# Performance work log

Hardware: AMD Instinct MI355X
Metric: run time of the kernel (lower is better)

## Reference

```python
import jax, jax.numpy as jnp
import numpy as np

T = 4096          # flattened document length (tokens)
FLAT = 512        # 2 * lstm_hidden_size
HD = 256          # head embedding dim (head_emb + char_emb)
FEAT = 20         # feature_size
MAXW = 20         # max mention width
NCAND = 30000     # enumerated candidate spans
HID = 512         # scorer hidden size
K = 1638          # floor(T * ment_ratio=0.4)
C = 40            # max antecedents
DEPTH = 2         # coref_depth
NSPK = 10
MENT = 2 * FLAT + FEAT + HD        # 1300 mention emb size
BIN_WIDTHS = [1, 1, 1, 1, 1, 4, 8, 16, 32]   # sums to 65 -> covers clamp(dist,0,64)
BINS = jnp.asarray(np.concatenate([np.full(w, i, dtype=np.int32) for i, w in enumerate(BIN_WIDTHS)]))


def _scorer(x, w1, b1, w2, b2, w3, b3):
    h = jax.nn.relu(x @ w1 + b1)
    h = jax.nn.relu(h @ w2 + b2)
    return (h @ w3 + b3)[..., 0]


def setup_inputs():
    key = jax.random.key(0)
    ks = jax.random.split(key, 30)
    p = lambda i, s: jax.random.normal(ks[i], s, jnp.float32) * 0.02
    cand_starts = jax.random.randint(ks[25], (NCAND,), 0, T)
    widths = jax.random.randint(ks[26], (NCAND,), 0, MAXW)
    cand_ends = jnp.minimum(cand_starts + widths, T - 1)
    return {
        "flat_lstm_out": jax.random.normal(ks[0], (T, FLAT), jnp.float32),
        "head_doc_embs": jax.random.normal(ks[1], (T, HD), jnp.float32),
        "w_span_head": p(2, (FLAT,)), "b_span_head": jnp.zeros((), jnp.float32),
        "width_embed": p(3, (MAXW, FEAT)),
        "ms_w1": p(4, (MENT, HID)), "ms_b1": jnp.zeros((HID,), jnp.float32),
        "ms_w2": p(5, (HID, HID)), "ms_b2": jnp.zeros((HID,), jnp.float32),
        "ms_w3": p(6, (HID, 1)), "ms_b3": jnp.zeros((1,), jnp.float32),
        "fast_w": p(7, (MENT, MENT)), "fast_b": jnp.zeros((MENT,), jnp.float32),
        "ss_w1": p(8, (3 * MENT + 3 * FEAT, HID)), "ss_b1": jnp.zeros((HID,), jnp.float32),
        "ss_w2": p(9, (HID, HID)), "ss_b2": jnp.zeros((HID,), jnp.float32),
        "ss_w3": p(10, (HID, 1)), "ss_b3": jnp.zeros((1,), jnp.float32),
        "gate_w": p(11, (2 * MENT, MENT)), "gate_b": jnp.zeros((MENT,), jnp.float32),
        "speaker_embed": p(12, (2, FEAT)),
        "genre_embed": p(13, (7, FEAT)),
        "dist_embed": p(14, (len(BIN_WIDTHS), FEAT)),
        "cand_starts": cand_starts,
        "cand_ends": cand_ends,
        "speaker_ids": jax.random.randint(ks[27], (T,), 0, NSPK),
        "genre_id": 3,
    }


def reference(flat_lstm_out, head_doc_embs, w_span_head, b_span_head, width_embed,
              ms_w1, ms_b1, ms_w2, ms_b2, ms_w3, ms_b3, fast_w, fast_b,
              ss_w1, ss_b1, ss_w2, ss_b2, ss_w3, ss_b3, gate_w, gate_b,
              speaker_embed, genre_embed, dist_embed,
              cand_starts, cand_ends, speaker_ids, genre_id):
    neg = -jnp.inf
    # ---- mention (span) embeddings: start/end gather + width emb + attention-pooled head ----
    width = cand_ends - cand_starts + 1                              # [N]
    start_embs = flat_lstm_out[cand_starts]                          # [N,FLAT]
    end_embs = flat_lstm_out[cand_ends]                              # [N,FLAT]
    width_embs = width_embed[width - 1]                              # [N,FEAT]
    span_idxs = jnp.clip(jnp.arange(MAXW)[None, :] + cand_starts[:, None], 0, T - 1)  # [N,W]
    ment_doc = head_doc_embs[span_idxs]                              # [N,W,HD]
    head_scores = flat_lstm_out @ w_span_head + b_span_head          # [T]
    g = head_scores[span_idxs] + jnp.where(jnp.arange(MAXW)[None, :] < width[:, None], 0.0, neg)
    attn = jax.nn.softmax(g, axis=1)                                 # [N,W]
    head_embs = jnp.einsum('nw,nwd->nd', attn, ment_doc)             # [N,HD]
    cand_embs = jnp.concatenate([start_embs, end_embs, width_embs, head_embs], axis=1)  # [N,MENT]
    cand_scores = _scorer(cand_embs, ms_w1, ms_b1, ms_w2, ms_b2, ms_w3, ms_b3)          # [N]
    # ---- prune mentions: top-k by score, reordered by document position ----
    _, top_idx = jax.lax.top_k(cand_scores, K)
    ment_pos = cand_starts[top_idx] * cand_ends[-1] + cand_ends[top_idx]
    top_idx = top_idx[jnp.argsort(ment_pos)]
    ment_embs = cand_embs[top_idx]                                   # [K,MENT]
    ment_scores = cand_scores[top_idx]                               # [K]
    ment_speakers = speaker_ids[cand_starts[top_idx]]                # [K]
    # ---- fast (bilinear) antecedent scoring + top-c pruning ----
    idx = jnp.arange(K)
    mask = (idx[:, None] - idx[None, :]) > 0                         # antecedent must precede
    src = ment_embs @ fast_w + fast_b
    fast = src @ ment_embs.T + ment_scores[:, None] + ment_scores[None, :] + jnp.where(mask, 0.0, neg)
    top_fast, antes = jax.lax.top_k(fast, C)                         # [K,C]
    dummy = jnp.zeros((K, 1), fast.dtype)
    genre_emb = jnp.broadcast_to(genre_embed[genre_id][None, None, :], (K, C, FEAT))
    ante_scores = top_fast
    # ---- iterative slow antecedent scoring + gated refinement ----
    for _ in range(DEPTH):
        ante_ment = ment_embs[antes]                                 # [K,C,MENT]
        same = (ment_speakers[:, None] == ment_speakers[antes]).astype(jnp.int32)
        spk_emb = speaker_embed[same]                                # [K,C,FEAT]
        dist_bin = BINS[jnp.clip(idx[:, None] - antes, 0, 64)]
        dist_emb = dist_embed[dist_bin]                              # [K,C,FEAT]
        me = jnp.broadcast_to(ment_embs[:, None, :], (K, C, MENT))
        ante_emb = jnp.concatenate([me, ante_ment, ante_ment * me, spk_emb, genre_emb, dist_emb], axis=2)
        ante_scores = top_fast + _scorer(ante_emb, ss_w1, ss_b1, ss_w2, ss_b2, ss_w3, ss_b3)
        weights = jax.nn.softmax(jnp.concatenate([dummy, ante_scores], axis=1), axis=-1)  # [K,C+1]
        stacked = jnp.concatenate([ment_embs[:, None, :], ante_ment], axis=1)             # [K,C+1,MENT]
        attended = jnp.einsum('kc,kcd->kd', weights, stacked)
        f = jax.nn.sigmoid(jnp.concatenate([ment_embs, attended], axis=1) @ gate_w + gate_b)
        ment_embs = f * attended + (1.0 - f) * ment_embs
    return jnp.concatenate([dummy, ante_scores], axis=1)             # [K,C+1] coref logits
```

## Files before the change

### kernel.cpp

```cpp
#include <hip/hip_runtime.h>
#include <math.h>

#define T_LEN 4096
#define FLATD 512
#define HDD 256
#define FEATD 20
#define NCAND 30000
#define HIDD 512
#define KSEL 1638
#define CANT 40
#define MENTD 1300
#define KPAD 1312
#define NPAIR (KSEL*CANT)
#define NEG_INF (-__builtin_inff())

#define MF_RELU 1
#define MF_MASK 4
#define MF_GATE 8

typedef unsigned short u16;
typedef __attribute__((ext_vector_type(8))) short bf16x8;
typedef __attribute__((ext_vector_type(4))) float f32x4;

__device__ __forceinline__ unsigned ordf(float f){
  unsigned u = __float_as_uint(f);
  return (u & 0x80000000u) ? ~u : (u | 0x80000000u);
}
__device__ __forceinline__ float unordf(unsigned u){
  return __uint_as_float((u & 0x80000000u) ? (u ^ 0x80000000u) : ~u);
}
__device__ __forceinline__ float bf2f(u16 h){ return __uint_as_float(((unsigned)h) << 16); }
__device__ __forceinline__ u16 f2bf(float f){
  unsigned u = __float_as_uint(f);
  u += 0x7fffu + ((u >> 16) & 1u);
  return (u16)(u >> 16);
}
__device__ __forceinline__ unsigned pkmul(unsigned a, unsigned b){
  float a0 = __uint_as_float(a << 16), a1 = __uint_as_float(a & 0xffff0000u);
  float b0 = __uint_as_float(b << 16), b1 = __uint_as_float(b & 0xffff0000u);
  float p0 = a0*b0, p1 = a1*b1;
  unsigned r;
  asm("v_cvt_pk_bf16_f32 %0, %1, %2" : "=v"(r) : "v"(p0), "v"(p1));
  return r;
}
__device__ __forceinline__ int featsrc(int k){
  if (k < 1024) return k;
  if (k < 1280) return k + 20;
  if (k < 1300) return k - 256;
  return -1;
}
__device__ __forceinline__ int swz(int row, int k8){
  return row*32 + ((k8 ^ ((row >> 1) & 3)) << 3);
}
__device__ __forceinline__ void gload16(const u16* g, u16* l){
  __builtin_amdgcn_global_load_lds((const __attribute__((address_space(1))) void*)(g),
                                   (__attribute__((address_space(3))) void*)(l), 16, 0, 0);
}

__global__ __launch_bounds__(256) void k_prep(const float* __restrict__ flat,
    const float* __restrict__ wemb, const float* __restrict__ fast_b, const float* __restrict__ gate_b,
    u16* __restrict__ flatbf, u16* __restrict__ wembP, float* __restrict__ fbP, float* __restrict__ gbP,
    unsigned* __restrict__ selws)
{
  int i = blockIdx.x*256 + threadIdx.x;
  if (i < T_LEN*FLATD) flatbf[i] = f2bf(flat[i]);
  if (i < 20*32) wembP[i] = ((i & 31) < 20) ? f2bf(wemb[(i >> 5)*FEATD + (i & 31)]) : (u16)0;
  if (i < KPAD){
    int s = featsrc(i);
    fbP[i] = (s >= 0) ? fast_b[s] : 0.f;
    gbP[i] = (s >= 0) ? gate_b[s] : 0.f;
  }
  if (i < 6156) selws[i] = 0;
}

__global__ __launch_bounds__(256) void k_head(const float* __restrict__ flat,
    const float* __restrict__ w, const float* __restrict__ b, float* __restrict__ hs)
{
  int lane = threadIdx.x & 63, wid = threadIdx.x >> 6;
  int row = blockIdx.x*4 + wid;
  if (row >= T_LEN) return;
  const float* x = flat + (size_t)row*FLATD;
  float s = 0.f;
  for (int j = lane; j < FLATD; j += 64) s += x[j]*w[j];
  #pragma unroll
  for (int o = 32; o; o >>= 1) s += __shfl_down(s, o, 64);
  if (lane == 0) hs[row] = s + b[0];
}

__global__ __launch_bounds__(256) void k_cand(const float* __restrict__ hs,
    const float* __restrict__ hdoc, const int* __restrict__ starts, const int* __restrict__ ends,
    u16* __restrict__ hemb)
{
  int wid = threadIdx.x >> 6, lane = threadIdx.x & 63;
  int n = blockIdx.x*4 + wid;
  if (n >= NCAND) return;
  int s = starts[n], e = ends[n];
  int width = e - s + 1;
  float g[20];
  #pragma unroll
  for (int w2 = 0; w2 < 20; ++w2) g[w2] = (w2 < width) ? hs[min(s + w2, T_LEN-1)] : NEG_INF;
  float m = NEG_INF;
  #pragma unroll
  for (int w2 = 0; w2 < 20; ++w2) m = fmaxf(m, g[w2]);
  float sum = 0.f;
  #pragma unroll
  for (int w2 = 0; w2 < 20; ++w2){ g[w2] = expf(g[w2] - m); sum += g[w2]; }
  float inv = 1.f/sum;
  #pragma unroll
  for (int di = 0; di < 4; ++di){
    int d = lane + di*64;
    float acc = 0.f;
    #pragma unroll
    for (int w2 = 0; w2 < 20; ++w2)
      acc += g[w2]*hdoc[(size_t)min(s + w2, T_LEN-1)*HDD + d];
    hemb[(size_t)n*HDD + d] = f2bf(acc*inv);
  }
}

__global__ __launch_bounds__(256) void k_transall(const float* __restrict__ ms_w1,
    const float* __restrict__ ms_w2, const float* __restrict__ fast_w,
    const float* __restrict__ ss_w1, const float* __restrict__ ss_w2,
    const float* __restrict__ gate_w,
    u16* ms1T, u16* ms2T, u16* fastT, u16* ss1abT, u16* sspT,
    u16* ss2T, u16* gateTall)
{
  const float* B; u16* D; int Kb, N, srcN, ldD, kperm, nperm;
  switch (blockIdx.z){
    case 0: B = ms_w1; D = ms1T; Kb = KPAD; N = HIDD; srcN = HIDD; ldD = KPAD; kperm = 1; nperm = 0; break;
    case 1: B = ms_w2; D = ms2T; Kb = HIDD; N = HIDD; srcN = HIDD; ldD = HIDD; kperm = 0; nperm = 0; break;
    case 2: B = fast_w; D = fastT; Kb = KPAD; N = MENTD; srcN = MENTD; ldD = KPAD; kperm = 1; nperm = 1; break;
    case 3: B = ss_w1; D = ss1abT; Kb = KPAD; N = HIDD; srcN = HIDD; ldD = KPAD; kperm = 1; nperm = 0; break;
    case 4: B = ss_w1 + (size_t)MENTD*HIDD; D = ss1abT + (size_t)512*KPAD; Kb = KPAD; N = HIDD; srcN = HIDD; ldD = KPAD; kperm = 1; nperm = 0; break;
    case 5: B = ss_w1 + (size_t)2*MENTD*HIDD; D = sspT; Kb = KPAD; N = HIDD; srcN = HIDD; ldD = KPAD; kperm = 1; nperm = 0; break;
    case 6: B = ss_w2; D = ss2T; Kb = HIDD; N = HIDD; srcN = HIDD; ldD = HIDD; kperm = 0; nperm = 0; break;
    case 7: B = gate_w; D = gateTall; Kb = KPAD; N = MENTD; srcN = MENTD; ldD = 2*KPAD; kperm = 1; nperm = 1; break;
    default: B = gate_w + (size_t)MENTD*MENTD; D = gateTall + KPAD; Kb = KPAD; N = MENTD; srcN = MENTD; ldD = 2*KPAD; kperm = 1; nperm = 1; break;
  }
  int k0 = blockIdx.x*32, n0 = blockIdx.y*32;
  if (k0 >= Kb || n0 >= N) return;
  __shared__ float t[32][33];
  int tx = threadIdx.x & 31, ty = threadIdx.x >> 5;
  for (int r = ty; r < 32; r += 8){
    int gk = k0 + r, gn = n0 + tx;
    int sk = kperm ? featsrc(gk) : ((gk < Kb) ? gk : -1);
    int sn = nperm ? ((gn < N) ? featsrc(gn) : -1) : ((gn < N) ? gn : -1);
    t[r][tx] = (sk >= 0 && sn >= 0) ? B[(size_t)sk*srcN + sn] : 0.f;
  }
  __syncthreads();
  for (int r = ty; r < 32; r += 8){
    int gn = n0 + r, gk = k0 + tx;
    if (gn < N && gk < Kb) D[(size_t)gn*ldD + gk] = f2bf(t[tx][r]);
  }
}

__global__ __launch_bounds__(256) void k_mfma_cand(
    const u16* __restrict__ flatbf, const u16* __restrict__ hemb, const u16* __restrict__ wembP,
    const int* __restrict__ starts, const int* __restrict__ ends,
    const u16* __restrict__ Bt, int M, const float* __restrict__ bias, u16* __restrict__ Cbf)
{
  __shared__ alignas(16) u16 As[4096];
  __shared__ alignas(16) u16 Bs[4096];
  int tid = threadIdx.x;
  int row0 = blockIdx.y*128, col0 = blockIdx.x*128;
  int lane = tid & 63, wid = tid >> 6;
  int wr = wid >> 1, wc = wid & 1;
  int l15 = lane & 15, l4 = lane >> 4;

  int s0 = tid, s1 = tid + 256;
  int r0s = s0 >> 2, c0s = s0 & 3;
  int r1s = s1 >> 2, c1s = s1 & 3;
  int k80 = (c0s ^ ((r0s >> 1) & 3)) << 3;
  int k81 = (c1s ^ ((r1s >> 1) & 3)) << 3;
  int n0r = row0 + r0s; if (n0r >= M) n0r = M - 1;
  int n1r = row0 + r1s; if (n1r >= M) n1r = M - 1;
  int sA0 = starts[n0r], eA0 = ends[n0r];
  int sA1 = starts[n1r], eA1 = ends[n1r];
  const u16* bS0 = flatbf + (size_t)sA0*FLATD;
  const u16* bE0 = flatbf + (size_t)eA0*FLATD;
  const u16* bH0 = hemb + (size_t)n0r*HDD;
  const u16* bW0 = wembP + (eA0 - sA0)*32;
  const u16* bS1 = flatbf + (size_t)sA1*FLATD;
  const u16* bE1 = flatbf + (size_t)eA1*FLATD;
  const u16* bH1p = hemb + (size_t)n1r*HDD;
  const u16* bW1 = wembP + (eA1 - sA1)*32;
  const u16* pb0 = Bt + (size_t)(col0 + r0s)*KPAD + k80;
  const u16* pb1 = Bt + (size_t)(col0 + r1s)*KPAD + k81;
  u16* la0 = As + s0*8; u16* la1 = As + s1*8;
  u16* lb0 = Bs + s0*8; u16* lb1 = Bs + s1*8;

  f32x4 acc[4][4];
  #pragma unroll
  for (int m = 0; m < 4; ++m)
    #pragma unroll
    for (int n = 0; n < 4; ++n)
      #pragma unroll
      for (int q = 0; q < 4; ++q) acc[m][n][q] = 0.f;

  for (int kt = 0; kt < KPAD/32; ++kt){
    int k0 = kt << 5;
    int f0 = k0 + k80, f1 = k0 + k81;
    const u16* src0 = (f0 < 512) ? bS0 + f0 : (f0 < 1024) ? bE0 + (f0 - 512)
                    : (f0 < 1280) ? bH0 + (f0 - 1024) : bW0 + (f0 - 1280);
    const u16* src1 = (f1 < 512) ? bS1 + f1 : (f1 < 1024) ? bE1 + (f1 - 512)
                    : (f1 < 1280) ? bH1p + (f1 - 1024) : bW1 + (f1 - 1280);
    gload16(src0, la0); gload16(src1, la1);
    gload16(pb0 + k0, lb0); gload16(pb1 + k0, lb1);
    __syncthreads();
    bf16x8 af[4], bfr[4];
    #pragma unroll
    for (int m = 0; m < 4; ++m){ int r = wr*64 + m*16 + l15; af[m] = *(const bf16x8*)(As + swz(r, l4)); }
    #pragma unroll
    for (int n = 0; n < 4; ++n){ int cc = wc*64 + n*16 + l15; bfr[n] = *(const bf16x8*)(Bs + swz(cc, l4)); }
    #pragma unroll
    for (int m = 0; m < 4; ++m)
      #pragma unroll
      for (int n = 0; n < 4; ++n)
        acc[m][n] = __builtin_amdgcn_mfma_f32_16x16x32_bf16(af[m], bfr[n], acc[m][n], 0, 0, 0);
    __syncthreads();
  }
  #pragma unroll
  for (int m = 0; m < 4; ++m){
    #pragma unroll
    for (int q = 0; q < 4; ++q){
      int grow = row0 + wr*64 + m*16 + l4*4 + q;
      if (grow >= M) continue;
      #pragma unroll
      for (int n = 0; n < 4; ++n){
        int gcol = col0 + wc*64 + n*16 + l15;
        float v = fmaxf(acc[m][n][q] + bias[gcol], 0.f);
        Cbf[(size_t)grow*HIDD + gcol] = f2bf(v);
      }
    }
  }
}

__global__ __launch_bounds__(256) void k_mfma(const u16* __restrict__ A,
    const u16* __restrict__ A2, const u16* __restrict__ Bt, int M, int N, int Kp, int ldA,
    const float* __restrict__ bias, const float* __restrict__ msc,
    float* __restrict__ Cf, int ldf, u16* __restrict__ Cbf, int ldbf, int Nstore, int flags,
    const u16* __restrict__ g_att, const u16* __restrict__ g_mo)
{
  __shared__ alignas(16) u16 As[4096];
  __shared__ alignas(16) u16 Bs[4096];
  int tid = threadIdx.x;
  int row0 = blockIdx.y*128, col0 = blockIdx.x*128;
  if ((flags & MF_MASK) && col0 >= row0 + 128) return;
  int lane = tid & 63, wid = tid >> 6;
  int wr = wid >> 1, wc = wid & 1;
  int l15 = lane & 15, l4 = lane >> 4;

  int s0 = tid, s1 = tid + 256;
  int r0s = s0 >> 2, c0s = s0 & 3;
  int r1s = s1 >> 2, c1s = s1 & 3;
  int k80 = (c0s ^ ((r0s >> 1) & 3)) << 3;
  int k81 = (c1s ^ ((r1s >> 1) & 3)) << 3;
  int ra0 = row0 + r0s; if (ra0 >= M) ra0 = M - 1;
  int ra1 = row0 + r1s; if (ra1 >= M) ra1 = M - 1;
  int cb0 = col0 + r0s; if (cb0 >= N) cb0 = N - 1;
  int cb1 = col0 + r1s; if (cb1 >= N) cb1 = N - 1;
  const u16* pa0 = A + (size_t)ra0*ldA + k80;
  const u16* pa1 = A + (size_t)ra1*ldA + k81;
  int kt1 = A2 ? (ldA >> 5) : (Kp >> 5);
  int koff = kt1 << 5;
  const u16* qa0 = A2 ? (A2 + (size_t)ra0*ldA + k80 - koff) : pa0;
  const u16* qa1 = A2 ? (A2 + (size_t)ra1*ldA + k81 - koff) : pa1;
  const u16* pb0 = Bt + (size_t)cb0*Kp + k80;
  const u16* pb1 = Bt + (size_t)cb1*Kp + k81;
  u16* la0 = As + s0*8; u16* la1 = As + s1*8;
  u16* lb0 = Bs + s0*8; u16* lb1 = Bs + s1*8;

  f32x4 acc[4][4];
  #pragma unroll
  for (int m = 0; m < 4; ++m)
    #pragma unroll
    for (int n = 0; n < 4; ++n)
      #pragma unroll
      for (int q = 0; q < 4; ++q) acc[m][n][q] = 0.f;

  int nkt = Kp >> 5;
  for (int kt = 0; kt < nkt; ++kt){
    int k0 = kt << 5;
    const u16* a0 = (kt < kt1) ? pa0 : qa0;
    const u16* a1 = (kt < kt1) ? pa1 : qa1;
    gload16(a0 + k0, la0); gload16(a1 + k0, la1);
    gload16(pb0 + k0, lb0); gload16(pb1 + k0, lb1);
    __syncthreads();
    bf16x8 af[4], bfr[4];
    #pragma unroll
    for (int m = 0; m < 4; ++m){ int r = wr*64 + m*16 + l15; af[m] = *(const bf16x8*)(As + swz(r, l4)); }
    #pragma unroll
    for (int n = 0; n < 4; ++n){ int cc = wc*64 + n*16 + l15; bfr[n] = *(const bf16x8*)(Bs + swz(cc, l4)); }
    #pragma unroll
    for (int m = 0; m < 4; ++m)
      #pragma unroll
      for (int n = 0; n < 4; ++n)
        acc[m][n] = __builtin_amdgcn_mfma_f32_16x16x32_bf16(af[m], bfr[n], acc[m][n], 0, 0, 0);
    __syncthreads();
  }
  #pragma unroll
  for (int m = 0; m < 4; ++m){
    #pragma unroll
    for (int q = 0; q < 4; ++q){
      int grow = row0 + wr*64 + m*16 + l4*4 + q;
      if (grow >= M) continue;
      #pragma unroll
      for (int n = 0; n < 4; ++n){
        int gcol = col0 + wc*64 + n*16 + l15;
        if (gcol < N){
          float v = acc[m][n][q];
          if (bias) v += bias[gcol];
          if (flags & MF_MASK){ v += msc[grow] + msc[gcol]; if (gcol >= grow) v = NEG_INF; }
          if (flags & MF_RELU) v = fmaxf(v, 0.f);
          if (flags & MF_GATE){
            float f = 1.f/(1.f + expf(-v));
            float res = f*bf2f(g_att[(size_t)grow*ldbf + gcol])
                      + (1.f - f)*bf2f(g_mo[(size_t)grow*ldbf + gcol]);
            Cbf[(size_t)grow*ldbf + gcol] = f2bf(res);
          } else {
            if (Cf)  Cf[(size_t)grow*ldf + gcol] = v;
            if (Cbf) Cbf[(size_t)grow*ldbf + gcol] = f2bf(v);
          }
        } else if (Cbf && gcol < Nstore){
          Cbf[(size_t)grow*ldbf + gcol] = 0;
        }
      }
    }
  }
}

__global__ __launch_bounds__(256) void k_mfma_rowdot(const u16* __restrict__ A,
    const u16* __restrict__ Bt, int M, const float* __restrict__ b2,
    const float* __restrict__ w3, const float* __restrict__ b3,
    const float* __restrict__ add, float* __restrict__ out)
{
  __shared__ alignas(16) u16 As[4096];
  __shared__ alignas(16) u16 Bs[4096];
  __shared__ float rsum[128][2];
  int tid = threadIdx.x;
  int row0 = blockIdx.x*128;
  int lane = tid & 63, wid = tid >> 6;
  int wr = wid >> 1, wc = wid & 1;
  int l15 = lane & 15, l4 = lane >> 4;

  int s0 = tid, s1 = tid + 256;
  int r0s = s0 >> 2, c0s = s0 & 3;
  int r1s = s1 >> 2, c1s = s1 & 3;
  int k80 = (c0s ^ ((r0s >> 1) & 3)) << 3;
  int k81 = (c1s ^ ((r1s >> 1) & 3)) << 3;
  int ra0 = row0 + r0s; if (ra0 >= M) ra0 = M - 1;
  int ra1 = row0 + r1s; if (ra1 >= M) ra1 = M - 1;
  const u16* pa0 = A + (size_t)ra0*HIDD + k80;
  const u16* pa1 = A + (size_t)ra1*HIDD + k81;
  u16* la0 = As + s0*8; u16* la1 = As + s1*8;
  u16* lb0 = Bs + s0*8; u16* lb1 = Bs + s1*8;

  float rd[4][4] = {};
  for (int p = 0; p < 4; ++p){
    int col0 = p*128;
    const u16* pb0 = Bt + (size_t)(col0 + r0s)*HIDD + k80;
    const u16* pb1 = Bt + (size_t)(col0 + r1s)*HIDD + k81;
    f32x4 acc[4][4];
    #pragma unroll
    for (int m = 0; m < 4; ++m)
      #pragma unroll
      for (int n = 0; n < 4; ++n)
        #pragma unroll
        for (int q = 0; q < 4; ++q) acc[m][n][q] = 0.f;
    for (int kt = 0; kt < HIDD/32; ++kt){
      int k0 = kt << 5;
      gload16(pa0 + k0, la0); gload16(pa1 + k0, la1);
      gload16(pb0 + k0, lb0); gload16(pb1 + k0, lb1);
      __syncthreads();
      bf16x8 af[4], bfr[4];
      #pragma unroll
      for (int m = 0; m < 4; ++m){ int r = wr*64 + m*16 + l15; af[m] = *(const bf16x8*)(As + swz(r, l4)); }
      #pragma unroll
      for (int n = 0; n < 4; ++n){ int cc = wc*64 + n*16 + l15; bfr[n] = *(const bf16x8*)(Bs + swz(cc, l4)); }
      #pragma unroll
      for (int m = 0; m < 4; ++m)
        #pragma unroll
        for (int n = 0; n < 4; ++n)
          acc[m][n] = __builtin_amdgcn_mfma_f32_16x16x32_bf16(af[m], bfr[n], acc[m][n], 0, 0, 0);
      __syncthreads();
    }
    #pragma unroll
    for (int n = 0; n < 4; ++n){
      int gcol = col0 + wc*64 + n*16 + l15;
      float bb = b2[gcol], ww = w3[gcol];
      #pragma unroll
      for (int m = 0; m < 4; ++m)
        #pragma unroll
        for (int q = 0; q < 4; ++q){
          float v = fmaxf(acc[m][n][q] + bb, 0.f);
          rd[m][q] = fmaf(v, ww, rd[m][q]);
        }
    }
  }
  #pragma unroll
  for (int m = 0; m < 4; ++m)
    #pragma unroll
    for (int q = 0; q < 4; ++q){
      float s = rd[m][q];
      s += __shfl_xor(s, 1, 64); s += __shfl_xor(s, 2, 64);
      s += __shfl_xor(s, 4, 64); s += __shfl_xor(s, 8, 64);
      if (l15 == 0) rsum[wr*64 + m*16 + l4*4 + q][wc] = s;
    }
  __syncthreads();
  if (tid < 128){
    int gr = row0 + tid;
    if (gr < M){
      float v = rsum[tid][0] + rsum[tid][1] + b3[0];
      if (add) v += add[gr];
      out[gr] = v;
    }
  }
}

__global__ __launch_bounds__(256) void k_d1_mfma(int Mc,
    const u16* __restrict__ ment, const int* __restrict__ antes, const int* __restrict__ mspk,
    const u16* __restrict__ Bt, const float* __restrict__ A_meb,
    const float* __restrict__ comb, u16* __restrict__ H1)
{
  __shared__ alignas(16) u16 As[4096];
  __shared__ alignas(16) u16 Bs[8192];
  __shared__ int ri[128], rj[128], rcomb[128];
  int tid = threadIdx.x;
  int row0 = blockIdx.y*128;
  int col0 = blockIdx.x*256;
  if (tid < 128){
    int r = row0 + tid;
    int p = (r < Mc ? r : 0);
    int i = p / CANT;
    int j = antes[p];
    ri[tid] = i; rj[tid] = j;
    int same = (mspk[i] == mspk[j]) ? 1 : 0;
    int d = i - j; d = d < 0 ? 0 : (d > 64 ? 64 : d);
    int bin = (d <= 4) ? d : (d <= 8 ? 5 : (d <= 16 ? 6 : (d <= 32 ? 7 : 8)));
    rcomb[tid] = same*9 + bin;
  }
  __syncthreads();
  int lane = tid & 63, wid = tid >> 6;
  int wr = wid >> 1, wc = wid & 1;
  int l15 = lane & 15, l4 = lane >> 4;

  int s0 = tid, s1 = tid + 256;
  int r0s = s0 >> 2, c0s = s0 & 3;
  int r1s = s1 >> 2, c1s = s1 & 3;
  int k80 = (c0s ^ ((r0s >> 1) & 3)) << 3;
  int k81 = (c1s ^ ((r1s >> 1) & 3)) << 3;
  const u16* pi0 = ment + (size_t)ri[r0s]*KPAD + k80;
  const u16* pj0 = ment + (size_t)rj[r0s]*KPAD + k80;
  const u16* pi1 = ment + (size_t)ri[r1s]*KPAD + k81;
  const u16* pj1 = ment + (size_t)rj[r1s]*KPAD + k81;
  int t0 = tid, t1 = tid + 256, t2 = tid + 512, t3 = tid + 768;
  int rB0 = t0 >> 2, rB1 = t1 >> 2, rB2 = t2 >> 2, rB3 = t3 >> 2;
  int kB0 = ((t0 & 3) ^ ((rB0 >> 1) & 3)) << 3;
  int kB1 = ((t1 & 3) ^ ((rB1 >> 1) & 3)) << 3;
  int kB2 = ((t2 & 3) ^ ((rB2 >> 1) & 3)) << 3;
  int kB3 = ((t3 & 3) ^ ((rB3 >> 1) & 3)) << 3;
  const u16* pb0 = Bt + (size_t)(col0 + rB0)*KPAD + kB0;
  const u16* pb1 = Bt + (size_t)(col0 + rB1)*KPAD + kB1;
  const u16* pb2 = Bt + (size_t)(col0 + rB2)*KPAD + kB2;
  const u16* pb3 = Bt + (size_t)(col0 + rB3)*KPAD + kB3;

  f32x4 acc[4][8];
  #pragma unroll
  for (int m = 0; m < 4; ++m)
    #pragma unroll
    for (int n = 0; n < 8; ++n)
      #pragma unroll
      for (int q = 0; q < 4; ++q) acc[m][n][q] = 0.f;

  uint4 va0 = *(const uint4*)pi0;
  uint4 vb0 = *(const uint4*)pj0;
  uint4 va1 = *(const uint4*)pi1;
  uint4 vb1 = *(const uint4*)pj1;

  int nkt = KPAD >> 5;
  for (int kt = 0; kt < nkt; ++kt){
    int k0 = kt << 5;
    {
      uint4 vo;
      vo.x = pkmul(va0.x, vb0.x); vo.y = pkmul(va0.y, vb0.y);
      vo.z = pkmul(va0.z, vb0.z); vo.w = pkmul(va0.w, vb0.w);
      *(uint4*)(As + s0*8) = vo;
      vo.x = pkmul(va1.x, vb1.x); vo.y = pkmul(va1.y, vb1.y);
      vo.z = pkmul(va1.z, vb1.z); vo.w = pkmul(va1.w, vb1.w);
      *(uint4*)(As + s1*8) = vo;
    }
    gload16(pb0 + k0, Bs + t0*8); gload16(pb1 + k0, Bs + t1*8);
    gload16(pb2 + k0, Bs + t2*8); gload16(pb3 + k0, Bs + t3*8);
    if (kt + 1 < nkt){
      int kn = (kt + 1) << 5;
      va0 = *(const uint4*)(pi0 + kn);
      vb0 = *(const uint4*)(pj0 + kn);
      va1 = *(const uint4*)(pi1 + kn);
      vb1 = *(const uint4*)(pj1 + kn);
    }
    __syncthreads();
    bf16x8 af[4];
    #pragma unroll
    for (int m = 0; m < 4; ++m){ int r = wr*64 + m*16 + l15; af[m] = *(const bf16x8*)(As + swz(r, l4)); }
    #pragma unroll
    for (int n = 0; n < 8; ++n){
      int cc = wc*128 + n*16 + l15;
      bf16x8 bfr = *(const bf16x8*)(Bs + swz(cc, l4));
      #pragma unroll
      for (int m = 0; m < 4; ++m)
        acc[m][n] = __builtin_amdgcn_mfma_f32_16x16x32_bf16(af[m], bfr, acc[m][n], 0, 0, 0);
    }
    __syncthreads();
  }
  #pragma unroll
  for (int m = 0; m < 4; ++m){
    #pragma unroll
    for (int q = 0; q < 4; ++q){
      int rl = wr*64 + m*16 + l4*4 + q;
      int grow = row0 + rl;
      if (grow >= Mc) continue;
      const float* me = A_meb + (size_t)ri[rl]*1024;
      const float* an = A_meb + (size_t)rj[rl]*1024 + 512;
      const float* cb = comb + (size_t)rcomb[rl]*HIDD;
      #pragma unroll
      for (int n = 0; n < 8; ++n){
        int gcol = col0 + wc*128 + n*16 + l15;
        float v = acc[m][n][q] + me[gcol] + an[gcol] + cb[gcol];
        H1[(size_t)grow*HIDD + gcol] = f2bf(fmaxf(v, 0.f));
      }
    }
  }
}

__global__ __launch_bounds__(256) void k_hist(const float* __restrict__ scores,
    unsigned* __restrict__ selws, int pass)
{
  int n = blockIdx.x*256 + threadIdx.x;
  if (n >= NCAND) return;
  unsigned u = ordf(scores[n]);
  const unsigned* meta = selws + 6144;
  if (pass == 0) atomicAdd(&selws[u >> 21], 1u);
  else if (pass == 1){ if ((u >> 21) == meta[0]) atomicAdd(&selws[2048 + ((u >> 10) & 0x7FFu)], 1u); }
  else { if ((u >> 10) == meta[2]) atomicAdd(&selws[4096 + (u & 0x3FFu)], 1u); }
}
__global__ __launch_bounds__(1024) void k_thresh(unsigned* __restrict__ selws, int mode){
  __shared__ unsigned a[2048], b[2048];
  int tid = threadIdx.x;
  unsigned* meta = selws + 6144;
  const unsigned* gbin = selws + (mode == 0 ? 0 : (mode == 1 ? 2048 : 4096));
  unsigned target = (mode == 0) ? (unsigned)KSEL : meta[mode == 1 ? 1 : 3];
  a[tid] = gbin[tid]; a[tid + 1024] = gbin[tid + 1024];
  unsigned *src = a, *dst = b;
  for (int step = 1; step < 2048; step <<= 1){
    __syncthreads();
    for (int i = tid; i < 2048; i += 1024)
      dst[i] = src[i] + ((i + step < 2048) ? src[i + step] : 0u);
    unsigned* t2 = src; src = dst; dst = t2;
  }
  __syncthreads();
  for (int i = tid; i < 2048; i += 1024){
    unsigned si = src[i], sn = (i < 2047) ? src[i+1] : 0u;
    if (si >= target && sn < target){
      if (mode == 0){ meta[0] = (unsigned)i; meta[1] = target - sn; }
// ... 32 lines not shown
__global__ __launch_bounds__(256) void k_rank1(const float* __restrict__ scores,
    const int* __restrict__ g_sel, int* __restrict__ ranked)
{
  __shared__ unsigned long long key[KSEL];
  int tid = threadIdx.x;
  for (int t = tid; t < KSEL; t += 256){
    int n = g_sel[t];
    key[t] = ((unsigned long long)(~ordf(scores[n])) << 32) | (unsigned)n;
  }
  __syncthreads();
  int t = blockIdx.x*256 + tid;
  if (t >= KSEL) return;
  unsigned long long mine = key[t];
  int r = 0;
  #pragma unroll 16
  for (int j = 0; j < KSEL; ++j) r += (key[j] < mine) ? 1 : 0;
  ranked[r] = (int)(mine & 0xFFFFFFFFu);
}
__global__ __launch_bounds__(256) void k_rank2(const int* __restrict__ ranked,
    const int* __restrict__ starts, const int* __restrict__ ends, int* __restrict__ top_idx)
{
  __shared__ unsigned long long key[KSEL];
  int tid = threadIdx.x;
  int elast = ends[NCAND-1];
  for (int t = tid; t < KSEL; t += 256){
    int n = ranked[t];
    unsigned mp = (unsigned)(starts[n]*elast + ends[n]);
    key[t] = ((unsigned long long)mp << 11) | (unsigned)t;
  }
  __syncthreads();
  int t = blockIdx.x*256 + tid;
  if (t >= KSEL) return;
  unsigned long long mine = key[t];
  int r = 0;
  #pragma unroll 16
  for (int j = 0; j < KSEL; ++j) r += (key[j] < mine) ? 1 : 0;
  top_idx[r] = ranked[t];
}

__global__ __launch_bounds__(256) void k_gather(const int* __restrict__ top_idx,
    const u16* __restrict__ flatbf, const u16* __restrict__ hemb, const u16* __restrict__ wembP,
    const int* __restrict__ starts, const int* __restrict__ ends,
    const float* __restrict__ cscores, const int* __restrict__ spk_ids,
    u16* __restrict__ ment, float* __restrict__ mscore, int* __restrict__ mspk)
{
  int k = blockIdx.x; int n = top_idx[k];
  int s = starts[n], e = ends[n];
  int v = threadIdx.x;
  if (v < KPAD/8){
    int f0 = v*8;
    const u16* src = (f0 < 512) ? flatbf + (size_t)s*FLATD + f0
                   : (f0 < 1024) ? flatbf + (size_t)e*FLATD + (f0 - 512)
                   : (f0 < 1280) ? hemb + (size_t)n*HDD + (f0 - 1024)
                   : wembP + (e - s)*32 + (f0 - 1280);
    *(uint4*)(ment + (size_t)k*KPAD + f0) = *(const uint4*)src;
  }
  if (threadIdx.x == 0){ mscore[k] = cscores[n]; mspk[k] = spk_ids[s]; }
}

__global__ __launch_bounds__(256) void k_f3(const float* __restrict__ fast,
    float* __restrict__ top_fast, int* __restrict__ antes)
{
  int wid = threadIdx.x >> 6, lane = threadIdx.x & 63;
  int i = blockIdx.x*4 + wid;
  if (i >= KSEL) return;
  const float* row = fast + (size_t)i*KSEL;
  unsigned long long key[26];
  #pragma unroll
  for (int t = 0; t < 26; ++t){
    int j = lane + (t << 6);
    unsigned long long k2 = 0ULL;
    if (j < i) k2 = ((unsigned long long)ordf(row[j]) << 32) | (unsigned)(0xFFFFFFFFu - (unsigned)j);
    key[t] = k2;
  }
  for (int c = 0; c < CANT; ++c){
    unsigned long long m = 0ULL;
    #pragma unroll
    for (int t = 0; t < 26; ++t) if (key[t] > m) m = key[t];
    #pragma unroll
    for (int o = 32; o; o >>= 1){
      unsigned long long v = __shfl_xor(m, o, 64);
      if (v > m) m = v;
    }
    if (m){
      #pragma unroll
      for (int t = 0; t < 26; ++t) if (key[t] == m) key[t] = 0ULL;
    }
    if (lane == 0){
      if (m){
        top_fast[(size_t)i*CANT + c] = unordf((unsigned)(m >> 32));
        antes[(size_t)i*CANT + c]    = (int)(0xFFFFFFFFu - (unsigned)(m & 0xFFFFFFFFu));
      } else {
        top_fast[(size_t)i*CANT + c] = NEG_INF;
        antes[(size_t)i*CANT + c]    = c;
      }
    }
  }
}

__global__ __launch_bounds__(256) void k_dsmall(const float* __restrict__ ss_w1,
    const float* __restrict__ ss_b1, const float* __restrict__ spk_emb,
    const float* __restrict__ gen_emb, const float* __restrict__ dist_emb,
    const int* __restrict__ genre_id, float* __restrict__ comb)
{
  int r = blockIdx.x;
  int same = r / 9, bin = r % 9;
  const float* es = spk_emb + same*FEATD;
// ... 72 lines not shown
  float v = (c == 0) ? 0.f : ante_sc[i*CANT + (c-1)];
  if (!isfinite(v)) v = -3.0e38f;
  out[idx] = v;
}

__global__ void k_zero(float* out, int n){
  int i = blockIdx.x*256 + threadIdx.x;
  if (i < n) out[i] = 0.f;
}

extern "C" void kernel_launch(void* const* d_in, const int* in_sizes, int n_in,
                              void* d_out, int out_size, void* d_ws, size_t ws_size,
                              hipStream_t stream)
{
  const float* flat   = (const float*)d_in[0];
  const float* hdoc   = (const float*)d_in[1];
  const float* w_head = (const float*)d_in[2];
  const float* b_head = (const float*)d_in[3];
  const float* wemb   = (const float*)d_in[4];
  const float* ms_w1  = (const float*)d_in[5];
  const float* ms_b1  = (const float*)d_in[6];
  const float* ms_w2  = (const float*)d_in[7];
  const float* ms_b2  = (const float*)d_in[8];
  const float* ms_w3  = (const float*)d_in[9];
  const float* ms_b3  = (const float*)d_in[10];
  const float* fast_w = (const float*)d_in[11];
  const float* fast_b = (const float*)d_in[12];
  const float* ss_w1  = (const float*)d_in[13];
  const float* ss_b1  = (const float*)d_in[14];
  const float* ss_w2  = (const float*)d_in[15];
  const float* ss_b2  = (const float*)d_in[16];
  const float* ss_w3  = (const float*)d_in[17];
  const float* ss_b3  = (const float*)d_in[18];
  const float* gate_w = (const float*)d_in[19];
  const float* gate_b = (const float*)d_in[20];
  const float* spk_e  = (const float*)d_in[21];
  const float* gen_e  = (const float*)d_in[22];
  const float* dist_e = (const float*)d_in[23];
  const int* starts   = (const int*)d_in[24];
  const int* ends     = (const int*)d_in[25];
  const int* spk_ids  = (const int*)d_in[26];
  const int* genre_id = (const int*)d_in[27];
  float* out = (float*)d_out;

  size_t off = 0;
  char* base = (char*)d_ws;
  auto alloc = [&](size_t nbytes) -> void* {
    void* p = (void*)(base + off);
    off += ((nbytes + 255)/256)*256;
    return p;
  };
  float* head_sc = (float*)alloc((size_t)T_LEN*4);
  u16*   flatbf  = (u16*)alloc((size_t)T_LEN*FLATD*2);
  u16*   wembP   = (u16*)alloc((size_t)20*32*2);
  float* fbP     = (float*)alloc((size_t)KPAD*4);
  float* gbP     = (float*)alloc((size_t)KPAD*4);
  u16*   hemb    = (u16*)alloc((size_t)NCAND*HDD*2);
  float* cscores = (float*)alloc((size_t)NCAND*4);
  int*   top_idx = (int*)alloc(2048*4);
  unsigned* selws= (unsigned*)alloc(6160*4);
  int*   g_sel   = (int*)alloc((size_t)KSEL*4);
  unsigned* g_eq = (unsigned*)alloc(1024*4);
  int*   g_rank  = (int*)alloc((size_t)KSEL*4);
  u16*   ms1T    = (u16*)alloc((size_t)HIDD*KPAD*2);
  u16*   ms2T    = (u16*)alloc((size_t)HIDD*HIDD*2);
  u16*   fastT   = (u16*)alloc((size_t)MENTD*KPAD*2);
  u16*   ss1abT  = (u16*)alloc((size_t)1024*KPAD*2);
  u16*   sspT    = (u16*)alloc((size_t)HIDD*KPAD*2);
  u16*   ss2T    = (u16*)alloc((size_t)HIDD*HIDD*2);
  u16*   gateTall= (u16*)alloc((size_t)MENTD*2*KPAD*2);
  u16*   ment    = (u16*)alloc((size_t)KSEL*KPAD*2);
  u16*   mentB   = (u16*)alloc((size_t)KSEL*KPAD*2);
  u16*   srcb    = (u16*)alloc((size_t)KSEL*KPAD*2);
  float* mscore  = (float*)alloc((size_t)KSEL*4);
  int*   mspk    = (int*)alloc((size_t)KSEL*4);
  float* fastm   = (float*)alloc((size_t)KSEL*KSEL*4);
  float* top_fast= (float*)alloc((size_t)NPAIR*4);
  int*   antes   = (int*)alloc((size_t)NPAIR*4);
  float* ante_sc = (float*)alloc((size_t)NPAIR*4);
  float* A_meb   = (float*)alloc((size_t)KSEL*1024*4);
  float* comb    = (float*)alloc((size_t)18*HIDD*4);
  u16*   att_bf  = (u16*)alloc((size_t)KSEL*KPAD*2);
  u16*   bufH1   = (u16*)alloc((size_t)NPAIR*HIDD*2);

  if (ws_size < off){
    k_zero<<<(KSEL*41 + 255)/256, 256, 0, stream>>>(out, KSEL*41);
    return;
  }

  k_prep<<<(T_LEN*FLATD + 255)/256, 256, 0, stream>>>(flat, wemb, fast_b, gate_b,
                                                      flatbf, wembP, fbP, gbP, selws);
  k_transall<<<dim3(KPAD/32, 41, 9), 256, 0, stream>>>(ms_w1, ms_w2, fast_w, ss_w1, ss_w2, gate_w,
      ms1T, ms2T, fastT, ss1abT, sspT, ss2T, gateTall);

  k_head<<<T_LEN/4, 256, 0, stream>>>(flat, w_head, b_head, head_sc);
  k_cand<<<NCAND/4, 256, 0, stream>>>(head_sc, hdoc, starts, ends, hemb);

  k_mfma_cand<<<dim3(HIDD/128, (NCAND + 127)/128), 256, 0, stream>>>(
      flatbf, hemb, wembP, starts, ends, ms1T, NCAND, ms_b1, bufH1);
  k_mfma_rowdot<<<(NCAND + 127)/128, 256, 0, stream>>>(bufH1, ms2T, NCAND, ms_b2, ms_w3, ms_b3,
                                                       nullptr, cscores);

  k_hist<<<(NCAND + 255)/256, 256, 0, stream>>>(cscores, selws, 0);
  k_thresh<<<1, 1024, 0, stream>>>(selws, 0);
  k_hist<<<(NCAND + 255)/256, 256, 0, stream>>>(cscores, selws, 1);
  k_thresh<<<1, 1024, 0, stream>>>(selws, 1);
  k_hist<<<(NCAND + 255)/256, 256, 0, stream>>>(cscores, selws, 2);
// ... 40 lines not shown
```

Measured before the change: 1.262 ms.

## Widen MFMA GEMM K-tile from 32 to 64 with new LDS swizzle

All bf16 MFMA GEMM kernels now stage a 64-wide K slice per iteration instead of 32, using a new 8-way XOR swizzle and doubling the LDS buffers. This halves the number of barrier pairs and global-to-LDS load rounds per GEMM. KPAD is raised to 1344 so K divides by 64, and the width-embedding table row stride becomes 64. The d1 kernel also drops its register prefetch of the next A tile and gains a launch_bounds occupancy hint. Costs are more LDS per block, which may lower occupancy, and about 2.4% more padded K work.

```diff
diff --git a/kernel.cpp b/kernel.cpp
--- a/kernel.cpp
+++ b/kernel.cpp
@@ -10,7 +10,7 @@
 #define KSEL 1638
 #define CANT 40
 #define MENTD 1300
-#define KPAD 1312
+#define KPAD 1344
 #define NPAIR (KSEL*CANT)
 #define NEG_INF (-__builtin_inff())
 
@@ -49,8 +49,11 @@
   if (k < 1300) return k - 256;
   return -1;
 }
-__device__ __forceinline__ int swz(int row, int k8){
-  return row*32 + ((k8 ^ ((row >> 1) & 3)) << 3);
+__device__ __forceinline__ int bsrc64(int S){
+  return (((S & 7) ^ ((S >> 3) & 7)) << 3);
+}
+__device__ __forceinline__ int brd64(int row, int h, int k8){
+  return row*64 + (((((h << 2) | k8)) ^ (row & 7)) << 3);
 }
 __device__ __forceinline__ void gload16(const u16* g, u16* l){
   __builtin_amdgcn_global_load_lds((const __attribute__((address_space(1))) void*)(g),
@@ -64,7 +67,7 @@
 {
   int i = blockIdx.x*256 + threadIdx.x;
   if (i < T_LEN*FLATD) flatbf[i] = f2bf(flat[i]);
-  if (i < 20*32) wembP[i] = ((i & 31) < 20) ? f2bf(wemb[(i >> 5)*FEATD + (i & 31)]) : (u16)0;
+  if (i < 20*64) wembP[i] = ((i & 63) < 20) ? f2bf(wemb[(i >> 6)*FEATD + (i & 63)]) : (u16)0;
   if (i < KPAD){
     int s = featsrc(i);
     fbP[i] = (s >= 0) ? fast_b[s] : 0.f;
@@ -158,35 +161,25 @@
     const int* __restrict__ starts, const int* __restrict__ ends,
     const u16* __restrict__ Bt, int M, const float* __restrict__ bias, u16* __restrict__ Cbf)
 {
-  __shared__ alignas(16) u16 As[4096];
-  __shared__ alignas(16) u16 Bs[4096];
+  __shared__ alignas(16) u16 As[8192];
+  __shared__ alignas(16) u16 Bs[8192];
   int tid = threadIdx.x;
   int row0 = blockIdx.y*128, col0 = blockIdx.x*128;
   int lane = tid & 63, wid = tid >> 6;
   int wr = wid >> 1, wc = wid & 1;
   int l15 = lane & 15, l4 = lane >> 4;
 
-  int s0 = tid, s1 = tid + 256;
-  int r0s = s0 >> 2, c0s = s0 & 3;
-  int r1s = s1 >> 2, c1s = s1 & 3;
-  int k80 = (c0s ^ ((r0s >> 1) & 3)) << 3;
-  int k81 = (c1s ^ ((r1s >> 1) & 3)) << 3;
-  int n0r = row0 + r0s; if (n0r >= M) n0r = M - 1;
-  int n1r = row0 + r1s; if (n1r >= M) n1r = M - 1;
-  int sA0 = starts[n0r], eA0 = ends[n0r];
-  int sA1 = starts[n1r], eA1 = ends[n1r];
-  const u16* bS0 = flatbf + (size_t)sA0*FLATD;
-  const u16* bE0 = flatbf + (size_t)eA0*FLATD;
-  const u16* bH0 = hemb + (size_t)n0r*HDD;
-  const u16* bW0 = wembP + (eA0 - sA0)*32;
-  const u16* bS1 = flatbf + (size_t)sA1*FLATD;
-  const u16* bE1 = flatbf + (size_t)eA1*FLATD;
-  const u16* bH1p = hemb + (size_t)n1r*HDD;
-  const u16* bW1 = wembP + (eA1 - sA1)*32;
-  const u16* pb0 = Bt + (size_t)(col0 + r0s)*KPAD + k80;
-  const u16* pb1 = Bt + (size_t)(col0 + r1s)*KPAD + k81;
-  u16* la0 = As + s0*8; u16* la1 = As + s1*8;
-  u16* lb0 = Bs + s0*8; u16* lb1 = Bs + s1*8;
+  int sS[4], eS[4], nS[4], so[4];
+  const u16* pb[4];
+  #pragma unroll
+  for (int i = 0; i < 4; ++i){
+    int S = tid + (i << 8);
+    int r = S >> 3;
+    so[i] = bsrc64(S);
+    int n = row0 + r; if (n >= M) n = M - 1;
+    sS[i] = starts[n]; eS[i] = ends[n]; nS[i] = n;
+    pb[i] = Bt + (size_t)(col0 + r)*KPAD + so[i];
+  }
 
   f32x4 acc[4][4];
   #pragma unroll
@@ -196,26 +189,32 @@
       #pragma unroll
       for (int q = 0; q < 4; ++q) acc[m][n][q] = 0.f;
 
-  for (int kt = 0; kt < KPAD/32; ++kt){
-    int k0 = kt << 5;
-    int f0 = k0 + k80, f1 = k0 + k81;
-    const u16* src0 = (f0 < 512) ? bS0 + f0 : (f0 < 1024) ? bE0 + (f0 - 512)
-                    : (f0 < 1280) ? bH0 + (f0 - 1024) : bW0 + (f0 - 1280);
-    const u16* src1 = (f1 < 512) ? bS1 + f1 : (f1 < 1024) ? bE1 + (f1 - 512)
-                    : (f1 < 1280) ? bH1p + (f1 - 1024) : bW1 + (f1 - 1280);
-    gload16(src0, la0); gload16(src1, la1);
-    gload16(pb0 + k0, lb0); gload16(pb1 + k0, lb1);
+  for (int kt = 0; kt < KPAD/64; ++kt){
+    int k0 = kt << 6;
+    #pragma unroll
+    for (int i = 0; i < 4; ++i){
+      int f = k0 + so[i];
+      const u16* src = (f < 512) ? flatbf + (size_t)sS[i]*FLATD + f
+                     : (f < 1024) ? flatbf + (size_t)eS[i]*FLATD + (f - 512)
+                     : (f < 1280) ? hemb + (size_t)nS[i]*HDD + (f - 1024)
+                     : wembP + (eS[i] - sS[i])*64 + (f - 1280);
+      gload16(src, As + (tid + (i << 8))*8);
+      gload16(pb[i] + k0, Bs + (tid + (i << 8))*8);
+    }
     __syncthreads();
-    bf16x8 af[4], bfr[4];
-    #pragma unroll
-    for (int m = 0; m < 4; ++m){ int r = wr*64 + m*16 + l15; af[m] = *(const bf16x8*)(As + swz(r, l4)); }
-    #pragma unroll
-    for (int n = 0; n < 4; ++n){ int cc = wc*64 + n*16 + l15; bfr[n] = *(const bf16x8*)(Bs + swz(cc, l4)); }
-    #pragma unroll
-    for (int m = 0; m < 4; ++m)
-      #pragma unroll
-      for (int n = 0; n < 4; ++n)
-        acc[m][n] = __builtin_amdgcn_mfma_f32_16x16x32_bf16(af[m], bfr[n], acc[m][n], 0, 0, 0);
+    #pragma unroll
+    for (int h = 0; h < 2; ++h){
+      bf16x8 af[4], bfr[4];
+      #pragma unroll
+      for (int m = 0; m < 4; ++m) af[m] = *(const bf16x8*)(As + brd64(wr*64 + m*16 + l15, h, l4));
+      #pragma unroll
+      for (int n = 0; n < 4; ++n) bfr[n] = *(const bf16x8*)(Bs + brd64(wc*64 + n*16 + l15, h, l4));
+      #pragma unroll
+      for (int m = 0; m < 4; ++m)
+        #pragma unroll
+        for (int n = 0; n < 4; ++n)
+          acc[m][n] = __builtin_amdgcn_mfma_f32_16x16x32_bf16(af[m], bfr[n], acc[m][n], 0, 0, 0);
+    }
     __syncthreads();
   }
   #pragma unroll
@@ -240,8 +239,8 @@
     float* __restrict__ Cf, int ldf, u16* __restrict__ Cbf, int ldbf, int Nstore, int flags,
     const u16* __restrict__ g_att, const u16* __restrict__ g_mo)
 {
-  __shared__ alignas(16) u16 As[4096];
-  __shared__ alignas(16) u16 Bs[4096];
+  __shared__ alignas(16) u16 As[8192];
+  __shared__ alignas(16) u16 Bs[8192];
   int tid = threadIdx.x;
   int row0 = blockIdx.y*128, col0 = blockIdx.x*128;
   if ((flags & MF_MASK) && col0 >= row0 + 128) return;
@@ -249,25 +248,20 @@
   int wr = wid >> 1, wc = wid & 1;
   int l15 = lane & 15, l4 = lane >> 4;
 
-  int s0 = tid, s1 = tid + 256;
-  int r0s = s0 >> 2, c0s = s0 & 3;
-  int r1s = s1 >> 2, c1s = s1 & 3;
-  int k80 = (c0s ^ ((r0s >> 1) & 3)) << 3;
-  int k81 = (c1s ^ ((r1s >> 1) & 3)) << 3;
-  int ra0 = row0 + r0s; if (ra0 >= M) ra0 = M - 1;
-  int ra1 = row0 + r1s; if (ra1 >= M) ra1 = M - 1;
-  int cb0 = col0 + r0s; if (cb0 >= N) cb0 = N - 1;
-  int cb1 = col0 + r1s; if (cb1 >= N) cb1 = N - 1;
-  const u16* pa0 = A + (size_t)ra0*ldA + k80;
-  const u16* pa1 = A + (size_t)ra1*ldA + k81;
-  int kt1 = A2 ? (ldA >> 5) : (Kp >> 5);
-  int koff = kt1 << 5;
-  const u16* qa0 = A2 ? (A2 + (size_t)ra0*ldA + k80 - koff) : pa0;
-  const u16* qa1 = A2 ? (A2 + (size_t)ra1*ldA + k81 - koff) : pa1;
-  const u16* pb0 = Bt + (size_t)cb0*Kp + k80;
-  const u16* pb1 = Bt + (size_t)cb1*Kp + k81;
-  u16* la0 = As + s0*8; u16* la1 = As + s1*8;
-  u16* lb0 = Bs + s0*8; u16* lb1 = Bs + s1*8;
+  const u16 *pa[4], *qa[4], *pb[4];
+  int kt1 = A2 ? (ldA >> 6) : (Kp >> 6);
+  int koff = kt1 << 6;
+  #pragma unroll
+  for (int i = 0; i < 4; ++i){
+    int S = tid + (i << 8);
+    int r = S >> 3;
+    int soi = bsrc64(S);
+    int ra = row0 + r; if (ra >= M) ra = M - 1;
+    int cb = col0 + r; if (cb >= N) cb = N - 1;
+    pa[i] = A + (size_t)ra*ldA + soi;
+    qa[i] = A2 ? (A2 + (size_t)ra*ldA + soi - koff) : pa[i];
+    pb[i] = Bt + (size_t)cb*Kp + soi;
+  }
 
   f32x4 acc[4][4];
   #pragma unroll
@@ -277,24 +271,29 @@
       #pragma unroll
       for (int q = 0; q < 4; ++q) acc[m][n][q] = 0.f;
 
-  int nkt = Kp >> 5;
+  int nkt = Kp >> 6;
   for (int kt = 0; kt < nkt; ++kt){
-    int k0 = kt << 5;
-    const u16* a0 = (kt < kt1) ? pa0 : qa0;
-    const u16* a1 = (kt < kt1) ? pa1 : qa1;
-    gload16(a0 + k0, la0); gload16(a1 + k0, la1);
-    gload16(pb0 + k0, lb0); gload16(pb1 + k0, lb1);
+    int k0 = kt << 6;
+    #pragma unroll
+    for (int i = 0; i < 4; ++i){
+      const u16* a = (kt < kt1) ? pa[i] : qa[i];
+      gload16(a + k0, As + (tid + (i << 8))*8);
+      gload16(pb[i] + k0, Bs + (tid + (i << 8))*8);
+    }
     __syncthreads();
-    bf16x8 af[4], bfr[4];
-    #pragma unroll
-    for (int m = 0; m < 4; ++m){ int r = wr*64 + m*16 + l15; af[m] = *(const bf16x8*)(As + swz(r, l4)); }
-    #pragma unroll
-    for (int n = 0; n < 4; ++n){ int cc = wc*64 + n*16 + l15; bfr[n] = *(const bf16x8*)(Bs + swz(cc, l4)); }
-    #pragma unroll
-    for (int m = 0; m < 4; ++m)
-      #pragma unroll
-      for (int n = 0; n < 4; ++n)
-        acc[m][n] = __builtin_amdgcn_mfma_f32_16x16x32_bf16(af[m], bfr[n], acc[m][n], 0, 0, 0);
+    #pragma unroll
+    for (int h = 0; h < 2; ++h){
+      bf16x8 af[4], bfr[4];
+      #pragma unroll
+      for (int m = 0; m < 4; ++m) af[m] = *(const bf16x8*)(As + brd64(wr*64 + m*16 + l15, h, l4));
+      #pragma unroll
+      for (int n = 0; n < 4; ++n) bfr[n] = *(const bf16x8*)(Bs + brd64(wc*64 + n*16 + l15, h, l4));
+      #pragma unroll
+      for (int m = 0; m < 4; ++m)
+        #pragma unroll
+        for (int n = 0; n < 4; ++n)
+          acc[m][n] = __builtin_amdgcn_mfma_f32_16x16x32_bf16(af[m], bfr[n], acc[m][n], 0, 0, 0);
+    }
     __syncthreads();
   }
   #pragma unroll
@@ -333,8 +332,8 @@
     const float* __restrict__ w3, const float* __restrict__ b3,
     const float* __restrict__ add, float* __restrict__ out)
 {
-  __shared__ alignas(16) u16 As[4096];
-  __shared__ alignas(16) u16 Bs[4096];
+  __shared__ alignas(16) u16 As[8192];
+  __shared__ alignas(16) u16 Bs[8192];
   __shared__ float rsum[128][2];
   int tid = threadIdx.x;
   int row0 = blockIdx.x*128;
@@ -342,23 +341,19 @@
   int wr = wid >> 1, wc = wid & 1;
   int l15 = lane & 15, l4 = lane >> 4;
 
-  int s0 = tid, s1 = tid + 256;
-  int r0s = s0 >> 2, c0s = s0 & 3;
-  int r1s = s1 >> 2, c1s = s1 & 3;
-  int k80 = (c0s ^ ((r0s >> 1) & 3)) << 3;
-  int k81 = (c1s ^ ((r1s >> 1) & 3)) << 3;
-  int ra0 = row0 + r0s; if (ra0 >= M) ra0 = M - 1;
-  int ra1 = row0 + r1s; if (ra1 >= M) ra1 = M - 1;
-  const u16* pa0 = A + (size_t)ra0*HIDD + k80;
-  const u16* pa1 = A + (size_t)ra1*HIDD + k81;
-  u16* la0 = As + s0*8; u16* la1 = As + s1*8;
-  u16* lb0 = Bs + s0*8; u16* lb1 = Bs + s1*8;
+  const u16* pa[4]; int so[4], rr[4];
+  #pragma unroll
+  for (int i = 0; i < 4; ++i){
+    int S = tid + (i << 8);
+    int r = S >> 3;
+    so[i] = bsrc64(S); rr[i] = r;
+    int ra = row0 + r; if (ra >= M) ra = M - 1;
+    pa[i] = A + (size_t)ra*HIDD + so[i];
+  }
 
   float rd[4][4] = {};
   for (int p = 0; p < 4; ++p){
     int col0 = p*128;
-    const u16* pb0 = Bt + (size_t)(col0 + r0s)*HIDD + k80;
-    const u16* pb1 = Bt + (size_t)(col0 + r1s)*HIDD + k81;
     f32x4 acc[4][4];
     #pragma unroll
     for (int m = 0; m < 4; ++m)
@@ -366,21 +361,27 @@
       for (int n = 0; n < 4; ++n)
         #pragma unroll
         for (int q = 0; q < 4; ++q) acc[m][n][q] = 0.f;
-    for (int kt = 0; kt < HIDD/32; ++kt){
-      int k0 = kt << 5;
-      gload16(pa0 + k0, la0); gload16(pa1 + k0, la1);
-      gload16(pb0 + k0, lb0); gload16(pb1 + k0, lb1);
+    for (int kt = 0; kt < HIDD/64; ++kt){
+      int k0 = kt << 6;
+      #pragma unroll
+      for (int i = 0; i < 4; ++i){
+        gload16(pa[i] + k0, As + (tid + (i << 8))*8);
+        gload16(Bt + (size_t)(col0 + rr[i])*HIDD + so[i] + k0, Bs + (tid + (i << 8))*8);
+      }
       __syncthreads();
-      bf16x8 af[4], bfr[4];
-      #pragma unroll
-      for (int m = 0; m < 4; ++m){ int r = wr*64 + m*16 + l15; af[m] = *(const bf16x8*)(As + swz(r, l4)); }
-      #pragma unroll
-      for (int n = 0; n < 4; ++n){ int cc = wc*64 + n*16 + l15; bfr[n] = *(const bf16x8*)(Bs + swz(cc, l4)); }
-      #pragma unroll
-      for (int m = 0; m < 4; ++m)
+      #pragma unroll
+      for (int h = 0; h < 2; ++h){
+        bf16x8 af[4], bfr[4];
         #pragma unroll
-        for (int n = 0; n < 4; ++n)
-          acc[m][n] = __builtin_amdgcn_mfma_f32_16x16x32_bf16(af[m], bfr[n], acc[m][n], 0, 0, 0);
+        for (int m = 0; m < 4; ++m) af[m] = *(const bf16x8*)(As + brd64(wr*64 + m*16 + l15, h, l4));
+        #pragma unroll
+        for (int n = 0; n < 4; ++n) bfr[n] = *(const bf16x8*)(Bs + brd64(wc*64 + n*16 + l15, h, l4));
+        #pragma unroll
+        for (int m = 0; m < 4; ++m)
+          #pragma unroll
+          for (int n = 0; n < 4; ++n)
+            acc[m][n] = __builtin_amdgcn_mfma_f32_16x16x32_bf16(af[m], bfr[n], acc[m][n], 0, 0, 0);
+      }
       __syncthreads();
     }
     #pragma unroll
@@ -416,13 +417,13 @@
   }
 }
 
-__global__ __launch_bounds__(256) void k_d1_mfma(int Mc,
+__global__ __launch_bounds__(256, 2) void k_d1_mfma(int Mc,
     const u16* __restrict__ ment, const int* __restrict__ antes, const int* __restrict__ mspk,
     const u16* __restrict__ Bt, const float* __restrict__ A_meb,
     const float* __restrict__ comb, u16* __restrict__ H1)
 {
-  __shared__ alignas(16) u16 As[4096];
-  __shared__ alignas(16) u16 Bs[8192];
+  __shared__ alignas(16) u16 As[8192];
+  __shared__ alignas(16) u16 Bs[16384];
   __shared__ int ri[128], rj[128], rcomb[128];
   int tid = threadIdx.x;
   int row0 = blockIdx.y*128;
@@ -443,25 +444,22 @@
   int wr = wid >> 1, wc = wid & 1;
   int l15 = lane & 15, l4 = lane >> 4;
 
-  int s0 = tid, s1 = tid + 256;
-  int r0s = s0 >> 2, c0s = s0 & 3;
-  int r1s = s1 >> 2, c1s = s1 & 3;
-  int k80 = (c0s ^ ((r0s >> 1) & 3)) << 3;
-  int k81 = (c1s ^ ((r1s >> 1) & 3)) << 3;
-  const u16* pi0 = ment + (size_t)ri[r0s]*KPAD + k80;
-  const u16* pj0 = ment + (size_t)rj[r0s]*KPAD + k80;
-  const u16* pi1 = ment + (size_t)ri[r1s]*KPAD + k81;
-  const u16* pj1 = ment + (size_t)rj[r1s]*KPAD + k81;
-  int t0 = tid, t1 = tid + 256, t2 = tid + 512, t3 = tid + 768;
-  int rB0 = t0 >> 2, rB1 = t1 >> 2, rB2 = t2 >> 2, rB3 = t3 >> 2;
-  int kB0 = ((t0 & 3) ^ ((rB0 >> 1) & 3)) << 3;
-  int kB1 = ((t1 & 3) ^ ((rB1 >> 1) & 3)) << 3;
-  int kB2 = ((t2 & 3) ^ ((rB2 >> 1) & 3)) << 3;
-  int kB3 = ((t3 & 3) ^ ((rB3 >> 1) & 3)) << 3;
-  const u16* pb0 = Bt + (size_t)(col0 + rB0)*KPAD + kB0;
-  const u16* pb1 = Bt + (size_t)(col0 + rB1)*KPAD + kB1;
-  const u16* pb2 = Bt + (size_t)(col0 + rB2)*KPAD + kB2;
-  const u16* pb3 = Bt + (size_t)(col0 + rB3)*KPAD + kB3;
+  const u16 *pi[4], *pj[4];
+  #pragma unroll
+  for (int i = 0; i < 4; ++i){
+    int S = tid + (i << 8);
+    int r = S >> 3;
+    int soi = bsrc64(S);
+    pi[i] = ment + (size_t)ri[r]*KPAD + soi;
+    pj[i] = ment + (size_t)rj[r]*KPAD + soi;
+  }
+  int bo[8];
+  #pragma unroll
+  for (int i = 0; i < 8; ++i){
+    int S = tid + (i << 8);
+    int r = S >> 3;
+    bo[i] = (col0 + r)*KPAD + bsrc64(S);
+  }
 
   f32x4 acc[4][8];
   #pragma unroll
@@ -471,43 +469,34 @@
       #pragma unroll
       for (int q = 0; q < 4; ++q) acc[m][n][q] = 0.f;
 
-  uint4 va0 = *(const uint4*)pi0;
-  uint4 vb0 = *(const uint4*)pj0;
-  uint4 va1 = *(const uint4*)pi1;
-  uint4 vb1 = *(const uint4*)pj1;
-
-  int nkt = KPAD >> 5;
+  int nkt = KPAD >> 6;
   for (int kt = 0; kt < nkt; ++kt){
-    int k0 = kt << 5;
-    {
+    int k0 = kt << 6;
+    #pragma unroll
+    for (int i = 0; i < 8; ++i)
+      gload16(Bt + bo[i] + k0, Bs + (tid + (i << 8))*8);
+    #pragma unroll
+    for (int i = 0; i < 4; ++i){
+      uint4 va = *(const uint4*)(pi[i] + k0);
+      uint4 vb = *(const uint4*)(pj[i] + k0);
       uint4 vo;
-      vo.x = pkmul(va0.x, vb0.x); vo.y = pkmul(va0.y, vb0.y);
-      vo.z = pkmul(va0.z, vb0.z); vo.w = pkmul(va0.w, vb0.w);
-      *(uint4*)(As + s0*8) = vo;
-      vo.x = pkmul(va1.x, vb1.x); vo.y = pkmul(va1.y, vb1.y);
-      vo.z = pkmul(va1.z, vb1.z); vo.w = pkmul(va1.w, vb1.w);
-      *(uint4*)(As + s1*8) = vo;
-    }
-    gload16(pb0 + k0, Bs + t0*8); gload16(pb1 + k0, Bs + t1*8);
-    gload16(pb2 + k0, Bs + t2*8); gload16(pb3 + k0, Bs + t3*8);
-    if (kt + 1 < nkt){
-      int kn = (kt + 1) << 5;
-      va0 = *(const uint4*)(pi0 + kn);
-      vb0 = *(const uint4*)(pj0 + kn);
-      va1 = *(const uint4*)(pi1 + kn);
-      vb1 = *(const uint4*)(pj1 + kn);
+      vo.x = pkmul(va.x, vb.x); vo.y = pkmul(va.y, vb.y);
+      vo.z = pkmul(va.z, vb.z); vo.w = pkmul(va.w, vb.w);
+      *(uint4*)(As + (tid + (i << 8))*8) = vo;
     }
     __syncthreads();
-    bf16x8 af[4];
-    #pragma unroll
-    for (int m = 0; m < 4; ++m){ int r = wr*64 + m*16 + l15; af[m] = *(const bf16x8*)(As + swz(r, l4)); }
-    #pragma unroll
-    for (int n = 0; n < 8; ++n){
-      int cc = wc*128 + n*16 + l15;
-      bf16x8 bfr = *(const bf16x8*)(Bs + swz(cc, l4));
-      #pragma unroll
-      for (int m = 0; m < 4; ++m)
-        acc[m][n] = __builtin_amdgcn_mfma_f32_16x16x32_bf16(af[m], bfr, acc[m][n], 0, 0, 0);
+    #pragma unroll
+    for (int h = 0; h < 2; ++h){
+      bf16x8 af[4];
+      #pragma unroll
+      for (int m = 0; m < 4; ++m) af[m] = *(const bf16x8*)(As + brd64(wr*64 + m*16 + l15, h, l4));
+      #pragma unroll
+      for (int n = 0; n < 8; ++n){
+        bf16x8 bfr = *(const bf16x8*)(Bs + brd64(wc*128 + n*16 + l15, h, l4));
+        #pragma unroll
+        for (int m = 0; m < 4; ++m)
+          acc[m][n] = __builtin_amdgcn_mfma_f32_16x16x32_bf16(af[m], bfr, acc[m][n], 0, 0, 0);
+      }
     }
     __syncthreads();
   }
@@ -646,7 +635,7 @@
     const u16* src = (f0 < 512) ? flatbf + (size_t)s*FLATD + f0
                    : (f0 < 1024) ? flatbf + (size_t)e*FLATD + (f0 - 512)
                    : (f0 < 1280) ? hemb + (size_t)n*HDD + (f0 - 1024)
-                   : wembP + (e - s)*32 + (f0 - 1280);
+                   : wembP + (e - s)*64 + (f0 - 1280);
     *(uint4*)(ment + (size_t)k*KPAD + f0) = *(const uint4*)src;
   }
   if (threadIdx.x == 0){ mscore[k] = cscores[n]; mspk[k] = spk_ids[s]; }
@@ -825,7 +814,7 @@
   };
   float* head_sc = (float*)alloc((size_t)T_LEN*4);
   u16*   flatbf  = (u16*)alloc((size_t)T_LEN*FLATD*2);
-  u16*   wembP   = (u16*)alloc((size_t)20*32*2);
+  u16*   wembP   = (u16*)alloc((size_t)20*64*2);
   float* fbP     = (float*)alloc((size_t)KPAD*4);
   float* gbP     = (float*)alloc((size_t)KPAD*4);
   u16*   hemb    = (u16*)alloc((size_t)NCAND*HDD*2);
```

Result: faster. 1.125 ms, median of 2 (-10.8%).
